# Kernel optimization log

Hardware: AMD Instinct MI355X
Metric: run time of the kernel (lower is better)

The kernel has to match this reference:

```python
import jax, jax.numpy as jnp
import numpy as np

N, A, C, S = 65536, 1024, 1000, 2  # S = max aug multiplier from self.augs


def _update_cv(x, labels, cov_prior, ave_prior, amount_prior):
    # Efficient segment-reduce form of update_CV (original builds O(N*C*A) onehot tensor)
    cnt = jax.ops.segment_sum(jnp.ones((N,), x.dtype), labels, num_segments=C)  # [C]
    sum_c = jax.ops.segment_sum(x, labels, num_segments=C)                      # [C,A]
    cnt_c = jnp.where(cnt == 0, 1.0, cnt)                                       # Amount_CxA clamp
    ave = sum_c / cnt_c[:, None]                                                # ave_CxA
    var = jax.ops.segment_sum((x - ave[labels]) ** 2, labels, num_segments=C) / cnt_c[:, None]
    var = jnp.where(var == 0, 1e-10, var)
    w = (cnt / (cnt + amount_prior + 1e-10))[:, None]                           # weight_CV [C,1]
    additional = w * (1 - w) * (ave_prior - ave) ** 2
    new_cov = cov_prior * (1 - w) + var * w + additional
    new_ave = ave_prior * (1 - w) + ave * w
    new_amount = amount_prior + cnt
    return new_cov, new_ave, new_amount


def setup_inputs() -> dict:
    key = jax.random.key(0)
    ks = jax.random.split(key, 6)
    return {
        "x": jax.random.normal(ks[0], (N, A), jnp.float32),
        "eps": jax.random.normal(ks[1], (S, C, A), jnp.float32),
        "fc_w": jax.random.normal(ks[2], (C, A), jnp.float32) * 0.02,
        "fc_b": jnp.zeros((C,), jnp.float32),
        "ba_coeffi": jax.random.normal(ks[3], (C,), jnp.float32) * 0.1,
        "cov_prior": jax.random.uniform(ks[4], (C, A), jnp.float32) * 0.01,
        "ave_prior": jnp.zeros((C, A), jnp.float32),
        "amount_prior": jnp.zeros((C,), jnp.float32),
        "target_x": jax.random.randint(ks[5], (N,), 0, C).astype(jnp.int64),
    }


def reference(x, eps, fc_w, fc_b, ba_coeffi, cov_prior, ave_prior, amount_prior, target_x):
    # update_CV runs under torch.no_grad -> stop_gradient on stats
    new_cov, new_ave, _ = _update_cv(x, target_x, cov_prior, ave_prior, amount_prior)
    new_cov = jax.lax.stop_gradient(new_cov)
    new_ave = jax.lax.stop_gradient(new_ave)
    # Gaussian augmentation: Normal(loc=Ave, scale=CoVariance).sample((S,)) per class
    aug = new_ave[None, :, :] + new_cov[None, :, :] * eps  # [S,C,A]
    aug = aug.reshape(S * C, A)
    aug_labels = jnp.tile(jnp.arange(C, dtype=target_x.dtype), S)
    feats = jnp.concatenate([x, aug], axis=0)              # [N+S*C, A]
    labels_all = jnp.concatenate([target_x, aug_labels], axis=0)
    logits = feats @ fc_w.T + fc_b - ba_coeffi             # [N+S*C, C]
    logp = jax.nn.log_softmax(logits, axis=-1)
    loss = -jnp.mean(jnp.take_along_axis(logp, labels_all[:, None], axis=1))
    return loss
```

## Files before the change

kernel.cpp:

```cpp
#include <hip/hip_runtime.h>

#define NROWS 65536
#define ADIM  1024
#define CCLS  1000
#define SAUG  2
#define MROWS (NROWS + SAUG*CCLS)
#define MPAD  67584
#define NPAD  1024
#define NPART 4
#define NEG_INF (-3.0e38f)

typedef __bf16 bf16x8 __attribute__((ext_vector_type(8)));
typedef float  f32x4  __attribute__((ext_vector_type(4)));
typedef unsigned short u16;

#define AS1 __attribute__((address_space(1)))
#define AS3 __attribute__((address_space(3)))

__device__ __forceinline__ unsigned pk2bf(float a, float b){
  unsigned ua = __float_as_uint(a), ub = __float_as_uint(b);
  ua = (ua + 0x7FFFu + ((ua>>16)&1u)) >> 16;
  ub = (ub + 0x7FFFu + ((ub>>16)&1u)) >> 16;
  return ua | (ub<<16);
}
__device__ __forceinline__ float bflo(unsigned u){ return __uint_as_float((u & 0xFFFFu) << 16); }
__device__ __forceinline__ float bfhi(unsigned u){ return __uint_as_float(u & 0xFFFF0000u); }

__global__ void k_hist(const int* __restrict__ tgt, int* __restrict__ cnt){
  int i = blockIdx.x*blockDim.x + threadIdx.x;
  int stride = gridDim.x*blockDim.x;
  for (; i < NROWS; i += stride) atomicAdd(&cnt[tgt[i]], 1);
}

__global__ void k_scan(const int* __restrict__ cnt, int* __restrict__ start){
  __shared__ int s[1024];
  int t = threadIdx.x;
  int v = (t < CCLS) ? cnt[t] : 0;
  s[t] = v;
  __syncthreads();
  for (int off = 1; off < 1024; off <<= 1){
    int u = (t >= off) ? s[t-off] : 0;
    __syncthreads();
    s[t] += u;
    __syncthreads();
  }
  if (t < CCLS) start[t] = s[t] - v;
}

__global__ void k_scatter(const int* __restrict__ tgt, const int* __restrict__ start,
                          int* __restrict__ pos, int* __restrict__ sorted){
  int i = blockIdx.x*blockDim.x + threadIdx.x;
  int stride = gridDim.x*blockDim.x;
  for (; i < NROWS; i += stride){
    int c = tgt[i];
    int r = atomicAdd(&pos[c], 1);
    sorted[start[c] + r] = i;
  }
}

__global__ void k_cvt_x(const float* __restrict__ x, u16* __restrict__ xb){
  size_t i = ((size_t)blockIdx.x*blockDim.x + threadIdx.x)*8;
  float4 a = *(const float4*)(x+i);
  float4 b = *(const float4*)(x+i+4);
  uint4 o;
  o.x = pk2bf(a.x,a.y); o.y = pk2bf(a.z,a.w);
  o.z = pk2bf(b.x,b.y); o.w = pk2bf(b.z,b.w);
  *(uint4*)(xb+i) = o;
}

__global__ void k_pad(u16* __restrict__ xb){
  size_t i = ((size_t)blockIdx.x*blockDim.x + threadIdx.x)*8 + (size_t)MROWS*ADIM;
  uint4 z = {0u,0u,0u,0u};
  *(uint4*)(xb+i) = z;
}

__global__ void k_cvt_w(const float* __restrict__ w, u16* __restrict__ wb){
  size_t i = ((size_t)blockIdx.x*blockDim.x + threadIdx.x)*8;
  int row = (int)(i >> 10);
  uint4 o = {0u,0u,0u,0u};
  if (row < CCLS){
    float4 a = *(const float4*)(w+i);
    float4 b = *(const float4*)(w+i+4);
    o.x = pk2bf(a.x,a.y); o.y = pk2bf(a.z,a.w);
    o.z = pk2bf(b.x,b.y); o.w = pk2bf(b.z,b.w);
  }
  *(uint4*)(wb+i) = o;
}

__global__ void k_bias(const float* __restrict__ fc_b, const float* __restrict__ ba,
                       float* __restrict__ biasv){
  int c = blockIdx.x*blockDim.x + threadIdx.x;
  if (c < NPAD) biasv[c] = (c < CCLS) ? fc_b[c] - ba[c] : NEG_INF;
}

__global__ void k_stats(const u16* __restrict__ xb_in, const int* __restrict__ sorted,
                        const int* __restrict__ cnt, const int* __restrict__ start,
                        const float* __restrict__ amt_p, const float* __restrict__ cov_p,
                        const float* __restrict__ ave_p, const float* __restrict__ eps,
                        u16* __restrict__ xb){
  __shared__ int sidx[256];
  int c = blockIdx.x;
  int t = threadIdx.x;
  int col = t*4;
  int n = cnt[c];
  int st = start[c];
  float s[4] = {0.f,0.f,0.f,0.f}, q[4] = {0.f,0.f,0.f,0.f};
  for (int base = 0; base < n; base += 256){
    int m = min(256, n - base);
    __syncthreads();
    if (t < m) sidx[t] = sorted[st + base + t];
    __syncthreads();
    int i = 0;
    for (; i + 4 <= m; i += 4){
      int r0 = sidx[i], r1 = sidx[i+1], r2 = sidx[i+2], r3 = sidx[i+3];
      uint2 u0 = *(const uint2*)(xb_in + (size_t)r0*ADIM + col);
      uint2 u1 = *(const uint2*)(xb_in + (size_t)r1*ADIM + col);
      uint2 u2 = *(const uint2*)(xb_in + (size_t)r2*ADIM + col);
      uint2 u3 = *(const uint2*)(xb_in + (size_t)r3*ADIM + col);
      {
        float v0=bflo(u0.x), v1=bfhi(u0.x), v2=bflo(u0.y), v3=bfhi(u0.y);
        s[0]+=v0; s[1]+=v1; s[2]+=v2; s[3]+=v3;
        q[0]+=v0*v0; q[1]+=v1*v1; q[2]+=v2*v2; q[3]+=v3*v3;
      }
      {
        float v0=bflo(u1.x), v1=bfhi(u1.x), v2=bflo(u1.y), v3=bfhi(u1.y);
        s[0]+=v0; s[1]+=v1; s[2]+=v2; s[3]+=v3;
        q[0]+=v0*v0; q[1]+=v1*v1; q[2]+=v2*v2; q[3]+=v3*v3;
      }
      {
        float v0=bflo(u2.x), v1=bfhi(u2.x), v2=bflo(u2.y), v3=bfhi(u2.y);
        s[0]+=v0; s[1]+=v1; s[2]+=v2; s[3]+=v3;
        q[0]+=v0*v0; q[1]+=v1*v1; q[2]+=v2*v2; q[3]+=v3*v3;
      }
      {
        float v0=bflo(u3.x), v1=bfhi(u3.x), v2=bflo(u3.y), v3=bfhi(u3.y);
        s[0]+=v0; s[1]+=v1; s[2]+=v2; s[3]+=v3;
        q[0]+=v0*v0; q[1]+=v1*v1; q[2]+=v2*v2; q[3]+=v3*v3;
      }
    }
    for (; i < m; i++){
      int row = sidx[i];
      const uint2 uv = *(const uint2*)(xb_in + (size_t)row*ADIM + col);
      float v0 = bflo(uv.x), v1 = bfhi(uv.x), v2 = bflo(uv.y), v3 = bfhi(uv.y);
      s[0]+=v0; s[1]+=v1; s[2]+=v2; s[3]+=v3;
      q[0]+=v0*v0; q[1]+=v1*v1; q[2]+=v2*v2; q[3]+=v3*v3;
    }
  }
  float cf = (float)n;
  float cc = (n == 0) ? 1.f : cf;
  float wgt = cf / (cf + amt_p[c] + 1e-10f);
  float4 cv = *(const float4*)(cov_p + (size_t)c*ADIM + col);
  float4 av = *(const float4*)(ave_p + (size_t)c*ADIM + col);
  float cvp[4] = {cv.x,cv.y,cv.z,cv.w};
  float avp[4] = {av.x,av.y,av.z,av.w};
  float ncov[4], nave[4];
  #pragma unroll
  for (int j = 0; j < 4; j++){
    float ave = s[j]/cc;
    float var = (q[j] - 2.f*ave*s[j] + cf*ave*ave)/cc;
    if (var <= 0.f) var = 1e-10f;
    float add = wgt*(1.f-wgt)*(avp[j]-ave)*(avp[j]-ave);
    ncov[j] = cvp[j]*(1.f-wgt) + var*wgt + add;
    nave[j] = avp[j]*(1.f-wgt) + ave*wgt;
  }
  #pragma unroll
  for (int s_ = 0; s_ < SAUG; s_++){
    size_t eoff = ((size_t)(s_*CCLS + c))*ADIM + col;
    size_t roff = ((size_t)(NROWS + s_*CCLS + c))*ADIM + col;
    const float4 e = *(const float4*)(eps + eoff);
    uint2 o;
    o.x = pk2bf(nave[0]+ncov[0]*e.x, nave[1]+ncov[1]*e.y);
    o.y = pk2bf(nave[2]+ncov[2]*e.z, nave[3]+ncov[3]*e.w);
    *(uint2*)(xb + roff) = o;
  }
}

__global__ __launch_bounds__(512,2) void k_gemm_part(
    const u16* __restrict__ xb, const u16* __restrict__ wb,
    const float* __restrict__ biasv, const int* __restrict__ tgt,
    float* __restrict__ pm, float* __restrict__ pl, float* __restrict__ plab){
  extern __shared__ char smem[];
  const int t = threadIdx.x;
  const int lane = t & 63;
  const int wv = t >> 6;
  const int wr = wv >> 2;
  const int wc = wv & 3;
  const int col = lane & 15;
  const int quad = lane >> 4;

  const int bid = blockIdx.x;
  const int wg  = (bid & 7)*132 + (bid >> 3);
  const int sp  = wg & 3;
  const int row0 = (wg >> 2) * 256;

  const unsigned lds0 = (unsigned)(size_t)((AS3 char*)smem);

  const unsigned swzq = (unsigned)((quad*16) ^ (((lane>>3)&1)*32));
  const unsigned vA0 = lds0 + (unsigned)((wr*128 + col)*64) + swzq;
  const unsigned vB0 = lds0 + 32768u + (unsigned)((wc*64 + col)*64) + swzq;
  const unsigned vA1 = vA0 + 65536u;
  const unsigned vB1 = vB0 + 65536u;

  const int ldsd = wv*1024;
  const int csw = ((lane&3)*8) ^ (((lane>>5)&1)*16);
  const int rT  = wv*16 + (lane>>2);
  const u16* pA = xb + (size_t)(row0 + rT)*ADIM + csw;
  const u16* pB = wb + (size_t)(sp*256 + rT)*ADIM + csw;

#define STG(PTR, DOFF, KOFF) do{ \
  __builtin_amdgcn_global_load_lds((const AS1 void*)((PTR) + (KOFF)), \
      (AS3 void*)(smem + (DOFF) + ldsd), 16, 0, 0); \
  __builtin_amdgcn_global_load_lds((const AS1 void*)((PTR) + (KOFF) + 131072), \
      (AS3 void*)(smem + (DOFF) + 8192 + ldsd), 16, 0, 0); \
}while(0)

#define DSR(dst, base, OFF) asm volatile("ds_read_b128 %0, %1 offset:" #OFF : "=v"(dst) : "v"(base))
#define RDA_K0LO(V) do{ DSR(a0,V,0);     DSR(a1,V,1024);  DSR(a2,V,2048);  DSR(a3,V,3072);  }while(0)
#define RDA_K0HI(V) do{ DSR(a0,V,4096);  DSR(a1,V,5120);  DSR(a2,V,6144);  DSR(a3,V,7168);  }while(0)
#define RDA_K1LO(V) do{ DSR(a0,V,16384); DSR(a1,V,17408); DSR(a2,V,18432); DSR(a3,V,19456); }while(0)
#define RDA_K1HI(V) do{ DSR(a0,V,20480); DSR(a1,V,21504); DSR(a2,V,22528); DSR(a3,V,23552); }while(0)
#define RDB_K0(V)   do{ DSR(b0,V,0);     DSR(b1,V,1024);  DSR(b2,V,2048);  DSR(b3,V,3072);  }while(0)
#define RDB_K1(V)   do{ DSR(b0,V,16384); DSR(b1,V,17408); DSR(b2,V,18432); DSR(b3,V,19456); }while(0)

#define MM(A_,B_,C_) C_ = __builtin_amdgcn_mfma_f32_16x16x32_bf16(A_,B_,C_,0,0,0)
#define MF16(MS) do{ \
  MM(a0,b0,acc[MS+0][0]); MM(a0,b1,acc[MS+0][1]); MM(a0,b2,acc[MS+0][2]); MM(a0,b3,acc[MS+0][3]); \
  MM(a1,b0,acc[MS+1][0]); MM(a1,b1,acc[MS+1][1]); MM(a1,b2,acc[MS+1][2]); MM(a1,b3,acc[MS+1][3]); \
  MM(a2,b0,acc[MS+2][0]); MM(a2,b1,acc[MS+2][1]); MM(a2,b2,acc[MS+2][2]); MM(a2,b3,acc[MS+2][3]); \
  MM(a3,b0,acc[MS+3][0]); MM(a3,b1,acc[MS+3][1]); MM(a3,b2,acc[MS+3][2]); MM(a3,b3,acc[MS+3][3]); \
}while(0)

#define VMW4 asm volatile("s_waitcnt vmcnt(4)" ::: "memory")
#define VMW0 asm volatile("s_waitcnt vmcnt(0)" ::: "memory")
#define BARMF(MS) do{ \
  __builtin_amdgcn_sched_barrier(0); \
  __builtin_amdgcn_s_barrier(); \
  asm volatile("s_waitcnt lgkmcnt(0)" ::: "memory"); \
  __builtin_amdgcn_sched_barrier(0); \
  __builtin_amdgcn_s_setprio(1); \
  MF16(MS); \
  __builtin_amdgcn_s_setprio(0); \
  __builtin_amdgcn_sched_barrier(0); \
  __builtin_amdgcn_s_barrier(); \
}while(0)

  f32x4 acc[8][4];
  const f32x4 z = {0.f,0.f,0.f,0.f};
  #pragma unroll
  for (int m = 0; m < 8; m++)
    #pragma unroll
    for (int n = 0; n < 4; n++) acc[m][n] = z;

  bf16x8 a0,a1,a2,a3,b0,b1,b2,b3;

  STG(pA, 0,      0);  STG(pB, 32768,  0);
  STG(pA, 16384,  32); STG(pB, 49152,  32);
  STG(pA, 65536,  64); STG(pB, 98304,  64);
  VMW0;
  __builtin_amdgcn_sched_barrier(0);
  __builtin_amdgcn_s_barrier();

  for (int it = 0; it < 7; it++){
    const int kb = it*128;
    RDA_K0LO(vA0); RDB_K0(vB0); STG(pA, 81920,  kb+96);  BARMF(0);
    RDA_K0HI(vA0);              STG(pB, 114688, kb+96);  VMW4; BARMF(4);
    RDA_K1LO(vA0); RDB_K1(vB0); STG(pA, 0,      kb+128); BARMF(0);
    RDA_K1HI(vA0);              STG(pB, 32768,  kb+128); BARMF(4);
    RDA_K0LO(vA1); RDB_K0(vB1); STG(pA, 16384,  kb+160); BARMF(0);
    RDA_K0HI(vA1);              STG(pB, 49152,  kb+160); VMW4; BARMF(4);
    RDA_K1LO(vA1); RDB_K1(vB1); STG(pA, 65536,  kb+192); BARMF(0);
    RDA_K1HI(vA1);              STG(pB, 98304,  kb+192); BARMF(4);
  }
  {
    RDA_K0LO(vA0); RDB_K0(vB0); STG(pA, 81920,  992);    BARMF(0);
    RDA_K0HI(vA0);              STG(pB, 114688, 992);    VMW4; BARMF(4);
    RDA_K1LO(vA0); RDB_K1(vB0);                          BARMF(0);
    RDA_K1HI(vA0);                                       BARMF(4);
    RDA_K0LO(vA1); RDB_K0(vB1);                          BARMF(0);
    RDA_K0HI(vA1);                                       VMW0; BARMF(4);
    RDA_K1LO(vA1); RDB_K1(vB1);                          BARMF(0);
    RDA_K1HI(vA1);                                       BARMF(4);
  }

#undef BARMF
#undef VMW0
#undef VMW4
#undef MF16
#undef MM
#undef RDB_K1
#undef RDB_K0
#undef RDA_K1HI
#undef RDA_K1LO
#undef RDA_K0HI
#undef RDA_K0LO
#undef DSR
#undef STG

  float bias[4];
  #pragma unroll
  for (int n = 0; n < 4; n++) bias[n] = biasv[sp*256 + wc*64 + n*16 + col];

  __syncthreads();
  float* red = (float*)smem;

  #pragma unroll
  for (int m = 0; m < 8; m++){
    #pragma unroll
    for (int rg = 0; rg < 4; rg++){
      const int rb = wr*128 + m*16 + quad*4 + rg;
      const int gr = row0 + rb;
      int lbl = -1;
      if (gr < NROWS) lbl = tgt[gr];
      else if (gr < MROWS){ int a_ = gr - NROWS; lbl = (a_ < CCLS) ? a_ : a_ - CCLS; }
      float lg[4];
      float mx = NEG_INF, lv = NEG_INF;
      #pragma unroll
      for (int n = 0; n < 4; n++){
        float v = acc[m][n][rg] + bias[n];
        lg[n] = v;
        mx = fmaxf(mx, v);
        int c = sp*256 + wc*64 + n*16 + col;
        lv = (c == lbl) ? v : lv;
      }
      #pragma unroll
      for (int o = 1; o < 16; o <<= 1) mx = fmaxf(mx, __shfl_xor(mx, o));
      float se = 0.f;
      #pragma unroll
      for (int n = 0; n < 4; n++) se += __expf(lg[n] - mx);
      #pragma unroll
      for (int o = 1; o < 16; o <<= 1) se += __shfl_xor(se, o);
      #pragma unroll
      for (int o = 1; o < 16; o <<= 1) lv = fmaxf(lv, __shfl_xor(lv, o));
      if (col == 0){
        red[0*1024 + rb*4 + wc] = mx;
        red[1*1024 + rb*4 + wc] = se;
        red[2*1024 + rb*4 + wc] = lv;
      }
    }
  }
  __syncthreads();
  if (t < 256){
    float m0 = red[t*4+0], m1 = red[t*4+1], m2 = red[t*4+2], m3 = red[t*4+3];
    float mx = fmaxf(fmaxf(m0,m1), fmaxf(m2,m3));
    float l  = red[1024+t*4+0]*__expf(m0-mx) + red[1024+t*4+1]*__expf(m1-mx)
             + red[1024+t*4+2]*__expf(m2-mx) + red[1024+t*4+3]*__expf(m3-mx);
    float lv = fmaxf(fmaxf(red[2048+t*4+0],red[2048+t*4+1]),
                     fmaxf(red[2048+t*4+2],red[2048+t*4+3]));
    size_t idx = (size_t)sp*MPAD + (size_t)(row0 + t);
    pm[idx]   = mx;
    pl[idx]   = l;
    plab[idx] = lv;
  }
}

__global__ void k_merge(const float* __restrict__ pm, const float* __restrict__ pl,
                        const float* __restrict__ plab, float* __restrict__ out){
  int r = blockIdx.x*256 + threadIdx.x;
  float v = 0.f;
  if (r < MROWS){
    float m = NEG_INF, lb = NEG_INF;
    #pragma unroll
    for (int s = 0; s < NPART; s++){
      m  = fmaxf(m,  pm[(size_t)s*MPAD + r]);
      lb = fmaxf(lb, plab[(size_t)s*MPAD + r]);
    }
    float l = 0.f;
    #pragma unroll
    for (int s = 0; s < NPART; s++)
      l += pl[(size_t)s*MPAD + r]*__expf(pm[(size_t)s*MPAD + r] - m);
    v = (m + __logf(l) - lb) * (1.0f/(float)MROWS);
  }
  #pragma unroll
  for (int o = 32; o > 0; o >>= 1) v += __shfl_xor(v, o);
  if ((threadIdx.x & 63) == 0) atomicAdd(out, v);
}

extern "C" void kernel_launch(void* const* d_in, const int* in_sizes, int n_in,
                              void* d_out, int out_size, void* d_ws, size_t ws_size,
                              hipStream_t stream) {
  const float* x     = (const float*)d_in[0];
  const float* eps   = (const float*)d_in[1];
  const float* fc_w  = (const float*)d_in[2];
  const float* fc_b  = (const float*)d_in[3];
  const float* ba    = (const float*)d_in[4];
  const float* cov_p = (const float*)d_in[5];
  const float* ave_p = (const float*)d_in[6];
  const float* amt_p = (const float*)d_in[7];
  const int*   tgt   = (const int*)d_in[8];
  float* out = (float*)d_out;

  char* ws = (char*)d_ws;
  u16*   xb    = (u16*)(ws);
  u16*   wb    = (u16*)(ws + 138412032u);
  float* biasv = (float*)(ws + 140509184u);
  int*   sorted= (int*)(ws + 140513280u);
  int*   cnt   = (int*)(ws + 140775424u);
  int*   pos   = (int*)(ws + 140779520u);
  int*   start = (int*)(ws + 140783616u);
  float* pm    = (float*)(ws + 140787712u);
  float* pl    = (float*)(ws + 142950400u);
  float* plab  = (float*)(ws + 145113088u);

  static int cfg = 0;
  if (!cfg){
    hipFuncSetAttribute((const void*)k_gemm_part,
                        hipFuncAttributeMaxDynamicSharedMemorySize, 131072);
    cfg = 1;
  }

  hipMemsetAsync(cnt, 0, 12288, stream);
  hipMemsetAsync(out, 0, sizeof(float), stream);

  k_hist   <<<256, 256, 0, stream>>>(tgt, cnt);
  k_scan   <<<1, 1024, 0, stream>>>(cnt, start);
  k_scatter<<<256, 256, 0, stream>>>(tgt, start, pos, sorted);
  k_cvt_x  <<<32768, 256, 0, stream>>>(x, xb);
  k_pad    <<<24, 256, 0, stream>>>(xb);
  k_cvt_w  <<<512, 256, 0, stream>>>(fc_w, wb);
  k_bias   <<<4, 256, 0, stream>>>(fc_b, ba, biasv);
  k_stats  <<<CCLS, 256, 0, stream>>>(xb, sorted, cnt, start, amt_p, cov_p, ave_p, eps, xb);
  k_gemm_part<<<1056, 512, 131072, stream>>>(xb, wb, biasv, tgt, pm, pl, plab);
  k_merge  <<<264, 256, 0, stream>>>(pm, pl, plab, out);
}
```

Measured before the change: 677.9 us.

## Double-buffer LDS fragments and cut barriers to two per K-block in GEMM mainloop

Restructures the GEMM main loop so LDS fragment reads for the next MFMA group go into a second register set while the current group's MFMAs run. Fine-grained lgkmcnt waits replace the full wait-plus-double-barrier around every MFMA group. Barriers drop from sixteen per iteration to two publish points, and the global-to-LDS staging order is reshuffled to fit. This uses more VGPRs for the extra fragment buffers and needs the reordered staging to stay race-free.

```diff
diff --git a/kernel.cpp b/kernel.cpp
--- a/kernel.cpp
+++ b/kernel.cpp
@@ -215,33 +215,30 @@
 }while(0)
 
 #define DSR(dst, base, OFF) asm volatile("ds_read_b128 %0, %1 offset:" #OFF : "=v"(dst) : "v"(base))
-#define RDA_K0LO(V) do{ DSR(a0,V,0);     DSR(a1,V,1024);  DSR(a2,V,2048);  DSR(a3,V,3072);  }while(0)
-#define RDA_K0HI(V) do{ DSR(a0,V,4096);  DSR(a1,V,5120);  DSR(a2,V,6144);  DSR(a3,V,7168);  }while(0)
-#define RDA_K1LO(V) do{ DSR(a0,V,16384); DSR(a1,V,17408); DSR(a2,V,18432); DSR(a3,V,19456); }while(0)
-#define RDA_K1HI(V) do{ DSR(a0,V,20480); DSR(a1,V,21504); DSR(a2,V,22528); DSR(a3,V,23552); }while(0)
-#define RDB_K0(V)   do{ DSR(b0,V,0);     DSR(b1,V,1024);  DSR(b2,V,2048);  DSR(b3,V,3072);  }while(0)
-#define RDB_K1(V)   do{ DSR(b0,V,16384); DSR(b1,V,17408); DSR(b2,V,18432); DSR(b3,V,19456); }while(0)
+#define RD4(D, V, O0,O1,O2,O3) do{ DSR(D[0],V,O0); DSR(D[1],V,O1); DSR(D[2],V,O2); DSR(D[3],V,O3); }while(0)
+
+#define LGKM(N) do{ \
+  asm volatile("s_waitcnt lgkmcnt(" #N ")" ::: "memory"); \
+  __builtin_amdgcn_sched_barrier(0); \
+}while(0)
 
 #define MM(A_,B_,C_) C_ = __builtin_amdgcn_mfma_f32_16x16x32_bf16(A_,B_,C_,0,0,0)
-#define MF16(MS) do{ \
-  MM(a0,b0,acc[MS+0][0]); MM(a0,b1,acc[MS+0][1]); MM(a0,b2,acc[MS+0][2]); MM(a0,b3,acc[MS+0][3]); \
-  MM(a1,b0,acc[MS+1][0]); MM(a1,b1,acc[MS+1][1]); MM(a1,b2,acc[MS+1][2]); MM(a1,b3,acc[MS+1][3]); \
-  MM(a2,b0,acc[MS+2][0]); MM(a2,b1,acc[MS+2][1]); MM(a2,b2,acc[MS+2][2]); MM(a2,b3,acc[MS+2][3]); \
-  MM(a3,b0,acc[MS+3][0]); MM(a3,b1,acc[MS+3][1]); MM(a3,b2,acc[MS+3][2]); MM(a3,b3,acc[MS+3][3]); \
+#define MFC(AS_,BS_,MS) do{ \
+  __builtin_amdgcn_s_setprio(1); \
+  MM(AS_[0],BS_[0],acc[(MS)+0][0]); MM(AS_[0],BS_[1],acc[(MS)+0][1]); MM(AS_[0],BS_[2],acc[(MS)+0][2]); MM(AS_[0],BS_[3],acc[(MS)+0][3]); \
+  MM(AS_[1],BS_[0],acc[(MS)+1][0]); MM(AS_[1],BS_[1],acc[(MS)+1][1]); MM(AS_[1],BS_[2],acc[(MS)+1][2]); MM(AS_[1],BS_[3],acc[(MS)+1][3]); \
+  MM(AS_[2],BS_[0],acc[(MS)+2][0]); MM(AS_[2],BS_[1],acc[(MS)+2][1]); MM(AS_[2],BS_[2],acc[(MS)+2][2]); MM(AS_[2],BS_[3],acc[(MS)+2][3]); \
+  MM(AS_[3],BS_[0],acc[(MS)+3][0]); MM(AS_[3],BS_[1],acc[(MS)+3][1]); MM(AS_[3],BS_[2],acc[(MS)+3][2]); MM(AS_[3],BS_[3],acc[(MS)+3][3]); \
+  __builtin_amdgcn_s_setprio(0); \
+  __builtin_amdgcn_sched_barrier(0); \
 }while(0)
 
-#define VMW4 asm volatile("s_waitcnt vmcnt(4)" ::: "memory")
-#define VMW0 asm volatile("s_waitcnt vmcnt(0)" ::: "memory")
-#define BARMF(MS) do{ \
+#define PUBLISH do{ \
+  asm volatile("s_waitcnt lgkmcnt(0)" ::: "memory"); \
+  asm volatile("s_waitcnt vmcnt(0)" ::: "memory"); \
   __builtin_amdgcn_sched_barrier(0); \
   __builtin_amdgcn_s_barrier(); \
-  asm volatile("s_waitcnt lgkmcnt(0)" ::: "memory"); \
   __builtin_amdgcn_sched_barrier(0); \
-  __builtin_amdgcn_s_setprio(1); \
-  MF16(MS); \
-  __builtin_amdgcn_s_setprio(0); \
-  __builtin_amdgcn_sched_barrier(0); \
-  __builtin_amdgcn_s_barrier(); \
 }while(0)
 
   f32x4 acc[8][4];
@@ -251,48 +248,75 @@
     #pragma unroll
     for (int n = 0; n < 4; n++) acc[m][n] = z;
 
-  bf16x8 a0,a1,a2,a3,b0,b1,b2,b3;
-
-  STG(pA, 0,      0);  STG(pB, 32768,  0);
-  STG(pA, 16384,  32); STG(pB, 49152,  32);
-  STG(pA, 65536,  64); STG(pB, 98304,  64);
-  VMW0;
+  bf16x8 A0[4], A1[4], B0[4], B1[4];
+
+  STG(pA, 0, 0);      STG(pA, 16384, 32);
+  STG(pB, 32768, 0);  STG(pB, 49152, 32);
+  STG(pA, 65536, 64); STG(pA, 81920, 96);
+  asm volatile("s_waitcnt vmcnt(4)" ::: "memory");
   __builtin_amdgcn_sched_barrier(0);
   __builtin_amdgcn_s_barrier();
+  __builtin_amdgcn_sched_barrier(0);
+  RD4(A0, vA0, 0,1024,2048,3072);
+  RD4(B0, vB0, 0,1024,2048,3072);
 
   for (int it = 0; it < 7; it++){
-    const int kb = it*128;
-    RDA_K0LO(vA0); RDB_K0(vB0); STG(pA, 81920,  kb+96);  BARMF(0);
-    RDA_K0HI(vA0);              STG(pB, 114688, kb+96);  VMW4; BARMF(4);
-    RDA_K1LO(vA0); RDB_K1(vB0); STG(pA, 0,      kb+128); BARMF(0);
-    RDA_K1HI(vA0);              STG(pB, 32768,  kb+128); BARMF(4);
-    RDA_K0LO(vA1); RDB_K0(vB1); STG(pA, 16384,  kb+160); BARMF(0);
-    RDA_K0HI(vA1);              STG(pB, 49152,  kb+160); VMW4; BARMF(4);
-    RDA_K1LO(vA1); RDB_K1(vB1); STG(pA, 65536,  kb+192); BARMF(0);
-    RDA_K1HI(vA1);              STG(pB, 98304,  kb+192); BARMF(4);
+    const int SA = it*128;
+    STG(pB, 98304, SA+64); STG(pB, 114688, SA+96);
+    RD4(A1, vA0, 4096,5120,6144,7168);
+    LGKM(4);  MFC(A0,B0,0);
+    RD4(A0, vA0, 16384,17408,18432,19456);
+    RD4(B1, vB0, 16384,17408,18432,19456);
+    LGKM(8);  MFC(A1,B0,4);
+    RD4(A1, vA0, 20480,21504,22528,23552);
+    LGKM(4);  MFC(A0,B1,0);
+    PUBLISH;
+    STG(pA, 0, SA+128); STG(pA, 16384, SA+160);
+    RD4(A0, vA1, 0,1024,2048,3072);
+    RD4(B0, vB1, 0,1024,2048,3072);
+    LGKM(8);  MFC(A1,B1,4);
+    STG(pB, 32768, SA+128); STG(pB, 49152, SA+160);
+    RD4(A1, vA1, 4096,5120,6144,7168);
+    LGKM(4);  MFC(A0,B0,0);
+    RD4(A0, vA1, 16384,17408,18432,19456);
+    RD4(B1, vB1, 16384,17408,18432,19456);
+    LGKM(8);  MFC(A1,B0,4);
+    RD4(A1, vA1, 20480,21504,22528,23552);
+    LGKM(4);  MFC(A0,B1,0);
+    PUBLISH;
+    STG(pA, 65536, SA+192); STG(pA, 81920, SA+224);
+    RD4(A0, vA0, 0,1024,2048,3072);
+    RD4(B0, vB0, 0,1024,2048,3072);
+    LGKM(8);  MFC(A1,B1,4);
   }
   {
-    RDA_K0LO(vA0); RDB_K0(vB0); STG(pA, 81920,  992);    BARMF(0);
-    RDA_K0HI(vA0);              STG(pB, 114688, 992);    VMW4; BARMF(4);
-    RDA_K1LO(vA0); RDB_K1(vB0);                          BARMF(0);
-    RDA_K1HI(vA0);                                       BARMF(4);
-    RDA_K0LO(vA1); RDB_K0(vB1);                          BARMF(0);
-    RDA_K0HI(vA1);                                       VMW0; BARMF(4);
-    RDA_K1LO(vA1); RDB_K1(vB1);                          BARMF(0);
-    RDA_K1HI(vA1);                                       BARMF(4);
-  }
-
-#undef BARMF
-#undef VMW0
-#undef VMW4
-#undef MF16
+    STG(pB, 98304, 960); STG(pB, 114688, 992);
+    RD4(A1, vA0, 4096,5120,6144,7168);
+    LGKM(4);  MFC(A0,B0,0);
+    RD4(A0, vA0, 16384,17408,18432,19456);
+    RD4(B1, vB0, 16384,17408,18432,19456);
+    LGKM(8);  MFC(A1,B0,4);
+    RD4(A1, vA0, 20480,21504,22528,23552);
+    LGKM(4);  MFC(A0,B1,0);
+    PUBLISH;
+    RD4(A0, vA1, 0,1024,2048,3072);
+    RD4(B0, vB1, 0,1024,2048,3072);
+    LGKM(8);  MFC(A1,B1,4);
+    RD4(A1, vA1, 4096,5120,6144,7168);
+    LGKM(4);  MFC(A0,B0,0);
+    RD4(A0, vA1, 16384,17408,18432,19456);
+    RD4(B1, vB1, 16384,17408,18432,19456);
+    LGKM(8);  MFC(A1,B0,4);
+    RD4(A1, vA1, 20480,21504,22528,23552);
+    LGKM(4);  MFC(A0,B1,0);
+    LGKM(0);  MFC(A1,B1,4);
+  }
+
+#undef PUBLISH
+#undef MFC
 #undef MM
-#undef RDB_K1
-#undef RDB_K0
-#undef RDA_K1HI
-#undef RDA_K1LO
-#undef RDA_K0HI
-#undef RDA_K0LO
+#undef LGKM
+#undef RD4
 #undef DSR
 #undef STG
 
```

Measured after the change: 659.3 us. -2.7%, faster.
